# Kernel optimization log

Measured on AMD Instinct MI355X. Metric: run time of the kernel, lower is better.

## Reference

```python
import jax, jax.numpy as jnp
import numpy as np

K = 8                   # num_RQS_bins
MIN_BW = 1e-6; MIN_BH = 1e-6; MIN_D = 1e-6
TAIL = 12.0             # tail_bound for 'linear' tails
# binary masks for num_inputs=4: kept (conditioning) dims and transformed dims per layer
MASK_IDX = [(0, 2), (1, 3), (0, 1), (2, 3)]
INV_IDX = [(1, 3), (0, 2), (2, 3), (0, 1)]


def _rqs_forward(x, uw, uh, ud):
    """Unconstrained rational-quadratic spline, forward (direct) pass.
    x: [B,F]; uw,uh: [B,F,K]; ud: [B,F,K-1]. Returns (y, logabsdet) each [B,F]."""
    const = float(np.log(np.exp(1.0 - MIN_D) - 1.0))
    ud = jnp.pad(ud, ((0, 0), (0, 0), (1, 1)), constant_values=const)  # [B,F,K+1]
    inside = (x >= -TAIL) & (x <= TAIL)
    xc = jnp.clip(x, -TAIL, TAIL)

    widths = MIN_BW + (1.0 - MIN_BW * K) * jax.nn.softmax(uw, -1)
    cumw = jnp.pad(jnp.cumsum(widths, -1), ((0, 0), (0, 0), (1, 0)))
    cumw = 2.0 * TAIL * cumw - TAIL
    cumw = cumw.at[..., 0].set(-TAIL).at[..., -1].set(TAIL)
    widths = cumw[..., 1:] - cumw[..., :-1]

    heights = MIN_BH + (1.0 - MIN_BH * K) * jax.nn.softmax(uh, -1)
    cumh = jnp.pad(jnp.cumsum(heights, -1), ((0, 0), (0, 0), (1, 0)))
    cumh = 2.0 * TAIL * cumh - TAIL
    cumh = cumh.at[..., 0].set(-TAIL).at[..., -1].set(TAIL)
    heights = cumh[..., 1:] - cumh[..., :-1]

    derivs = MIN_D + jax.nn.softplus(ud)  # [B,F,K+1]

    # searchsorted over bin edges (forward mode uses cumwidths)
    idx = jnp.clip(jnp.sum((xc[..., None] >= cumw).astype(jnp.int32), -1) - 1, 0, K - 1)
    g = lambda t: jnp.take_along_axis(t, idx[..., None], axis=-1)[..., 0]
    in_cw, in_w = g(cumw), g(widths)
    in_ch, in_h = g(cumh), g(heights)
    delta = in_h / in_w
    d_k, d_k1 = g(derivs), g(derivs[..., 1:])

    theta = (xc - in_cw) / in_w
    tomt = theta * (1.0 - theta)
    num = in_h * (delta * theta ** 2 + d_k * tomt)
    den = delta + (d_k + d_k1 - 2.0 * delta) * tomt
    y = in_ch + num / den
    dnum = delta ** 2 * (d_k1 * theta ** 2 + 2.0 * delta * tomt + d_k * (1.0 - theta) ** 2)
    lad = jnp.log(dnum) - 2.0 * jnp.log(den)

    return jnp.where(inside, y, x), jnp.where(inside, lad, 0.0)


def setup_inputs() -> dict:
    key = jax.random.key(0)
    ks = jax.random.split(key, 5)
    B, H = 262144, 128
    OM = 3 * K - 1  # 23 params per transformed dim
    inputs = jax.random.normal(ks[0], (B, 4), jnp.float32)
    cond_inputs = jax.random.uniform(ks[1], (B, 1), jnp.float32)
    W1 = jax.random.normal(ks[2], (4, H, 3), jnp.float32) / np.sqrt(3.0)
    b1 = jnp.zeros((4, H), jnp.float32)
    W2 = jax.random.normal(ks[3], (4, H, H), jnp.float32) / np.sqrt(float(H))
    b2 = jnp.zeros((4, H), jnp.float32)
    W3 = jax.random.normal(ks[4], (4, 2 * OM, H), jnp.float32) / np.sqrt(float(H))
    b3 = jnp.zeros((4, 2 * OM), jnp.float32)
    return {"inputs": inputs, "cond_inputs": cond_inputs,
            "W1": W1, "b1": b1, "W2": W2, "b2": b2, "W3": W3, "b3": b3}


def reference(inputs, cond_inputs, W1, b1, W2, b2, W3, b3):
    B = inputs.shape[0]
    x = inputs
    logdets = jnp.zeros((B, 1), dtype=inputs.dtype)
    for l in range(4):  # fixed small number of coupling layers
        midx = list(MASK_IDX[l]); iidx = list(INV_IDX[l])
        m_in = jnp.concatenate([x[:, midx], cond_inputs], -1)  # [B,3]
        h = jax.nn.relu(m_in @ W1[l].T + b1[l])
        h = jax.nn.relu(h @ W2[l].T + b2[l])
        params = h @ W3[l].T + b3[l]  # [B, F*(3K-1)]
        F = len(iidx)
        tp = jnp.swapaxes(params.reshape(B, 3 * K - 1, F), 1, 2)  # [B,F,3K-1]
        y, lad = _rqs_forward(x[:, iidx], tp[..., :K], tp[..., K:2 * K], tp[..., 2 * K:])
        x = x.at[:, iidx].set(y)
        logdets = logdets + jnp.sum(lad, -1, keepdims=True)
    return x, logdets
```

## Files before the change

### kernel.cpp

```cpp
#include <hip/hip_runtime.h>

#define TAILB 12.0f
#define INV2048 4.8828125e-4f

typedef _Float16 half8 __attribute__((ext_vector_type(8)));
typedef _Float16 half4 __attribute__((ext_vector_type(4)));
typedef __fp16 fp16x2 __attribute__((ext_vector_type(2)));
typedef __attribute__((ext_vector_type(4))) float f32x4;

#define MFMAH __builtin_amdgcn_mfma_f32_16x16x32_f16

#define WAVE_SYNC() do {                                  \
    __builtin_amdgcn_sched_barrier(0);                    \
    asm volatile("s_waitcnt lgkmcnt(0)" ::: "memory");    \
    __builtin_amdgcn_sched_barrier(0);                    \
} while (0)

__device__ __forceinline__ float softplus_f(float z) {
    return (z > 15.f) ? z : __logf(1.f + __expf(z));
}

__device__ __forceinline__ void split2h(float v, _Float16& o0, _Float16& o1) {
    _Float16 h0 = (_Float16)v;
    float r1 = v - (float)h0;
    o0 = h0;
    o1 = (_Float16)(r1 * 2048.0f);
}

__device__ __forceinline__ void split4_pk(const float* v, half4& p0, half4& p1) {
    fp16x2 lo = __builtin_amdgcn_cvt_pkrtz(v[0], v[1]);
    fp16x2 hi = __builtin_amdgcn_cvt_pkrtz(v[2], v[3]);
    float r0 = (v[0] - (float)lo.x) * 2048.f;
    float r1 = (v[1] - (float)lo.y) * 2048.f;
    float r2 = (v[2] - (float)hi.x) * 2048.f;
    float r3 = (v[3] - (float)hi.y) * 2048.f;
    fp16x2 rlo = __builtin_amdgcn_cvt_pkrtz(r0, r1);
    fp16x2 rhi = __builtin_amdgcn_cvt_pkrtz(r2, r3);
    p0 = (half4){(_Float16)lo.x, (_Float16)lo.y, (_Float16)hi.x, (_Float16)hi.y};
    p1 = (half4){(_Float16)rlo.x, (_Float16)rlo.y, (_Float16)rhi.x, (_Float16)rhi.y};
}

__global__ __launch_bounds__(256)
void prep_v15(const float* __restrict__ W1, const float* __restrict__ b1,
              const float* __restrict__ W2, const float* __restrict__ W3,
              _Float16* __restrict__ W2F, _Float16* __restrict__ W3F,
              float4* __restrict__ w1p)
{
    int id = blockIdx.x * 256 + threadIdx.x;
    if (id < 65536) {
        int j = id & 7, ln = (id >> 3) & 63, tile = id >> 9;
        int cs = tile & 3, t = (tile >> 2) & 1, wv = (tile >> 3) & 3, l = tile >> 5;
        int n = 32 * wv + 16 * t + (ln & 15);
        int k = 32 * cs + 8 * (ln >> 4) + j;
        _Float16 a, b;
        split2h(W2[l * 16384 + n * 128 + k], a, b);
        W2F[(tile * 2 + 0) * 512 + ln * 8 + j] = a;
        W2F[(tile * 2 + 1) * 512 + ln * 8 + j] = b;
    } else if (id < 90112) {
        int t2 = id - 65536;
        int j = t2 & 7, ln = (t2 >> 3) & 63, tile3 = t2 >> 9;
        int cs = tile3 & 3, q = tile3 >> 2;
        int wv = q % 3, l = q / 3;
        int p = 16 * wv + (ln & 15);
        int n = 32 * cs + 8 * (ln >> 4) + j;
        float v = (p < 46) ? W3[l * 5888 + p * 128 + n] : 0.f;
        _Float16 a, b;
        split2h(v, a, b);
        W3F[(tile3 * 2 + 0) * 512 + ln * 8 + j] = a;
        W3F[(tile3 * 2 + 1) * 512 + ln * 8 + j] = b;
    } else if (id < 90624) {
        int t = id - 90112;
        int l = t >> 7, k = t & 127;
        float4 v;
        v.x = W1[l * 384 + k * 3 + 0];
        v.y = W1[l * 384 + k * 3 + 1];
        v.z = W1[l * 384 + k * 3 + 2];
        v.w = b1[l * 128 + k];
        w1p[t] = v;
    }
}

__global__ __launch_bounds__(64, 2)
void rqs_v15(const float* __restrict__ inp, const float* __restrict__ cond,
             const _Float16* __restrict__ W2F, const _Float16* __restrict__ W3F,
             const float4* __restrict__ w1p,
             const float* __restrict__ b2, const float* __restrict__ b3,
             float* __restrict__ out, int B)
{
    __shared__ __align__(16) _Float16 planes[2][32][128];
    __shared__ float xbuf[32][5];

    char* plw = (char*)&planes[0][0][0];
    const char* pl = plw;

    const int ln   = threadIdx.x;
    const int base = blockIdx.x * 32;
    const int sm   = ln & 15;
    const int qd   = ln >> 4;
    const int s1   = ln & 31;
    const int hi   = ln >> 5;

    int rdaddr[2][4];
    #pragma unroll
    for (int st = 0; st < 2; ++st)
        #pragma unroll
        for (int cs = 0; cs < 4; ++cs)
            rdaddr[st][cs] = (16 * st + sm) * 256 + (((4 * cs + qd) ^ sm) << 4);
    const int wrb = s1 * 256 + hi * 8;

    if (ln < 32) {
        float4 xi = reinterpret_cast<const float4*>(inp)[base + ln];
        xbuf[ln][0] = xi.x; xbuf[ln][1] = xi.y;
        xbuf[ln][2] = xi.z; xbuf[ln][3] = xi.w;
        xbuf[ln][4] = cond[base + ln];
    }
    float ladreg = 0.f;
    WAVE_SYNC();

    #pragma unroll 1
    for (int l = 0; l < 4; ++l) {
        int mi0, mi1, ii0, ii1;
        switch (l) {
            case 0:  mi0 = 0; mi1 = 2; ii0 = 1; ii1 = 3; break;
            case 1:  mi0 = 1; mi1 = 3; ii0 = 0; ii1 = 2; break;
            case 2:  mi0 = 0; mi1 = 1; ii0 = 2; ii1 = 3; break;
            default: mi0 = 2; mi1 = 3; ii0 = 0; ii1 = 1; break;
        }

        {
            float m0 = xbuf[s1][mi0], m1 = xbuf[s1][mi1], cc = xbuf[s1][4];
            const float4* w1l = w1p + l * 128;
            #pragma unroll 4
            for (int g = 0; g < 16; ++g) {
                float v[4];
                #pragma unroll
                for (int j = 0; j < 4; ++j) {
                    float4 w4 = w1l[g * 8 + hi * 4 + j];
                    v[j] = fmaxf(fmaf(w4.x, m0, fmaf(w4.y, m1, fmaf(w4.z, cc, w4.w))), 0.f);
                }
                half4 p0, p1;
                split4_pk(v, p0, p1);
                char* wp = plw + wrb + ((g ^ sm) << 4);
                *(half4*)(wp)        = p0;
                *(half4*)(wp + 8192) = p1;
            }
        }
        WAVE_SYNC();

        half8 bf[2][4][2];
        #pragma unroll
        for (int st = 0; st < 2; ++st)
            #pragma unroll
            for (int cs = 0; cs < 4; ++cs) {
                bf[st][cs][0] = *(const half8*)(pl + rdaddr[st][cs]);
                bf[st][cs][1] = *(const half8*)(pl + rdaddr[st][cs] + 8192);
            }
        WAVE_SYNC();

        const half8* W2F8 = (const half8*)W2F;
        #pragma unroll 1
        for (int np = 0; np < 4; ++np) {
            f32x4 accA[2][2], accB[2][2];
            #pragma unroll
            for (int i = 0; i < 2; ++i) {
                float4 bias = *(const float4*)(b2 + l * 128 + (2 * np + i) * 16 + 4 * qd);
                #pragma unroll
                for (int st = 0; st < 2; ++st) {
                    accA[i][st] = (f32x4){bias.x, bias.y, bias.z, bias.w};
                    accB[i][st] = (f32x4){0.f, 0.f, 0.f, 0.f};
                }
            }
            #pragma unroll
            for (int cs = 0; cs < 4; ++cs) {
                #pragma unroll
                for (int i = 0; i < 2; ++i) {
                    int tile = l * 8 + 2 * np + i;
                    half8 A0 = W2F8[((tile * 4 + cs) * 2 + 0) * 64 + ln];
                    half8 A1 = W2F8[((tile * 4 + cs) * 2 + 1) * 64 + ln];
                    #pragma unroll
                    for (int st = 0; st < 2; ++st) {
                        accA[i][st] = MFMAH(A0, bf[st][cs][0], accA[i][st], 0, 0, 0);
                        accB[i][st] = MFMAH(A0, bf[st][cs][1], accB[i][st], 0, 0, 0);
                        accB[i][st] = MFMAH(A1, bf[st][cs][0], accB[i][st], 0, 0, 0);
                    }
                }
            }
            #pragma unroll
            for (int i = 0; i < 2; ++i) {
                int g = 2 * (2 * np + i) + (qd >> 1);
                #pragma unroll
                for (int st = 0; st < 2; ++st) {
                    float v[4];
                    #pragma unroll
                    for (int r = 0; r < 4; ++r)
                        v[r] = fmaxf(fmaf(INV2048, accB[i][st][r], accA[i][st][r]), 0.f);
                    half4 p0, p1;
                    split4_pk(v, p0, p1);
                    char* wp = plw + (16 * st + sm) * 256 + ((g ^ sm) << 4) + ((qd & 1) << 3);
                    *(half4*)(wp)        = p0;
                    *(half4*)(wp + 8192) = p1;
                }
            }
        }
        WAVE_SYNC();

        #pragma unroll
        for (int st = 0; st < 2; ++st)
            #pragma unroll
            for (int cs = 0; cs < 4; ++cs) {
                bf[st][cs][0] = *(const half8*)(pl + rdaddr[st][cs]);
                bf[st][cs][1] = *(const half8*)(pl + rdaddr[st][cs] + 8192);
            }
        WAVE_SYNC();

        const half8* W3F8 = (const half8*)W3F;
        #pragma unroll 1
        for (int pt = 0; pt < 3; ++pt) {
            f32x4 a3A[2], a3B[2];
            #pragma unroll
            for (int st = 0; st < 2; ++st) {
                a3A[st] = (f32x4){0.f, 0.f, 0.f, 0.f};
                a3B[st] = (f32x4){0.f, 0.f, 0.f, 0.f};
            }
            #pragma unroll
            for (int cs = 0; cs < 4; ++cs) {
                int q = (l * 3 + pt) * 4 + cs;
                half8 A0 = W3F8[(q * 2 + 0) * 64 + ln];
                half8 A1 = W3F8[(q * 2 + 1) * 64 + ln];
                #pragma unroll
                for (int st = 0; st < 2; ++st) {
                    a3A[st] = MFMAH(A0, bf[st][cs][0], a3A[st], 0, 0, 0);
                    a3B[st] = MFMAH(A0, bf[st][cs][1], a3B[st], 0, 0, 0);
                    a3B[st] = MFMAH(A1, bf[st][cs][0], a3B[st], 0, 0, 0);
                }
            }
            #pragma unroll
            for (int st = 0; st < 2; ++st) {
                float4 pv;
                pv.x = fmaf(INV2048, a3B[st][0], a3A[st][0]);
                pv.y = fmaf(INV2048, a3B[st][1], a3A[st][1]);
                pv.z = fmaf(INV2048, a3B[st][2], a3A[st][2]);
                pv.w = fmaf(INV2048, a3B[st][3], a3A[st][3]);
                *(float4*)(plw + (16 * st + sm) * 208 + (16 * pt + 4 * qd) * 4) = pv;
            }
        }
        WAVE_SYNC();

        {
            const float* b3l = b3 + l * 46;
            const float4* prow = (const float4*)(pl + s1 * 208);
            float pr[23];
            #pragma unroll
            for (int i = 0; i < 12; ++i) {
                float4 q = prow[i];
                pr[2 * i] = (hi ? q.y : q.x) + b3l[4 * i + hi];
                if (2 * i + 1 < 23)
                    pr[2 * i + 1] = (hi ? q.w : q.z) + b3l[4 * i + 2 + hi];
            }

            float xin = xbuf[s1][hi == 0 ? ii0 : ii1];

            float d[9];
            d[0] = 1.f; d[8] = 1.f;
            #pragma unroll
            for (int k = 1; k < 8; ++k) d[k] = 1e-6f + softplus_f(pr[16 + k - 1]);

            bool inside = (xin >= -TAILB) && (xin <= TAILB);
            float xc = fminf(fmaxf(xin, -TAILB), TAILB);

            float mw = pr[0], mh = pr[8];
            #pragma unroll
            for (int k = 1; k < 8; ++k) { mw = fmaxf(mw, pr[k]); mh = fmaxf(mh, pr[8 + k]); }
            float ew[8], eh[8], swm = 0.f, shm = 0.f;
            #pragma unroll
            for (int k = 0; k < 8; ++k) {
                ew[k] = __expf(pr[k] - mw);     swm += ew[k];
                eh[k] = __expf(pr[8 + k] - mh); shm += eh[k];
            }
            const float c1 = 1.f - 8e-6f;
            float isw = __fdividef(c1, swm), ish = __fdividef(c1, shm);

            float cum_w = 0.f, cum_h = 0.f;
            float cwk = -TAILB, chk = -TAILB;
            float s_cw = -TAILB, s_w = 2.f * TAILB, s_ch = -TAILB, s_h = 2.f * TAILB;
            float s_d0 = 1.f, s_d1 = d[1];
            #pragma unroll
            for (int k = 0; k < 8; ++k) {
                cum_w += fmaf(ew[k], isw, 1e-6f);
                cum_h += fmaf(eh[k], ish, 1e-6f);
                float cwn = (k == 7) ? TAILB : fmaf(2.f * TAILB, cum_w, -TAILB);
                float chn = (k == 7) ? TAILB : fmaf(2.f * TAILB, cum_h, -TAILB);
                bool ge = (xc >= cwk);
                s_cw = ge ? cwk : s_cw;  s_w = ge ? (cwn - cwk) : s_w;
                s_ch = ge ? chk : s_ch;  s_h = ge ? (chn - chk) : s_h;
                s_d0 = ge ? d[k] : s_d0; s_d1 = ge ? d[k + 1] : s_d1;
                cwk = cwn; chk = chn;
            }

            float rw    = __fdividef(1.f, s_w);
            float th    = (xc - s_cw) * rw;
            float delta = s_h * rw;
            float omt   = 1.f - th;
            float tomt  = th * omt;
            float num   = s_h * fmaf(delta, th * th, s_d0 * tomt);
            float den   = fmaf(s_d0 + s_d1 - 2.f * delta, tomt, delta);
            float y     = s_ch + __fdividef(num, den);
            float dnum  = delta * delta * (s_d1 * th * th + 2.f * delta * tomt + s_d0 * omt * omt);
            float lad   = __logf(dnum) - 2.f * __logf(den);

            xbuf[s1][hi == 0 ? ii0 : ii1] = inside ? y : xin;
            ladreg += inside ? lad : 0.f;
        }
        WAVE_SYNC();
    }

    float lsum = ladreg + __shfl(ladreg, (ln + 32) & 63, 64);
    if (ln < 32) {
        float4 xo;
        xo.x = xbuf[ln][0]; xo.y = xbuf[ln][1];
        xo.z = xbuf[ln][2]; xo.w = xbuf[ln][3];
        reinterpret_cast<float4*>(out)[base + ln] = xo;
        out[(size_t)B * 4 + base + ln] = lsum;
    }
}

extern "C" void kernel_launch(void* const* d_in, const int* in_sizes, int n_in,
                              void* d_out, int out_size, void* d_ws, size_t ws_size,
                              hipStream_t stream) {
    const float* inp  = (const float*)d_in[0];
    const float* cond = (const float*)d_in[1];
    const float* W1   = (const float*)d_in[2];
    const float* b1   = (const float*)d_in[3];
    const float* W2   = (const float*)d_in[4];
    const float* b2   = (const float*)d_in[5];
    const float* W3   = (const float*)d_in[6];
    const float* b3   = (const float*)d_in[7];
    float* out = (float*)d_out;
    int B = in_sizes[0] / 4;

    char* ws = (char*)d_ws;
    _Float16* W2F = (_Float16*)(ws);
    _Float16* W3F = (_Float16*)(ws + 262144);
    float4*   w1p = (float4*)(ws + 360448);

    hipLaunchKernelGGL(prep_v15, dim3(354), dim3(256), 0, stream,
                       W1, b1, W2, W3, W2F, W3F, w1p);
    hipLaunchKernelGGL(rqs_v15, dim3(B / 32), dim3(64), 0, stream,
                       inp, cond, W2F, W3F, w1p, b2, b3, out, B);
}
```

Baseline: 269.5 us.

## Halve LDS staging buffer by processing activations in K-halves, raise occupancy

The 16 KB activation staging buffer becomes 8 KB. The layer-1 output and the layer-2 output are each written and read back in two K-halves, using a row-based XOR swizzle over 128-byte rows. Layer-2 results go into a separate register fragment set (bf3), so the layer-1 fragments do not have to be reloaded. Launch bounds rise from 2 to 3 waves per SIMD to exploit the smaller LDS footprint, at the cost of more wave syncs and tighter register budgets that could cause spills.

```diff
diff --git a/kernel.cpp b/kernel.cpp
--- a/kernel.cpp
+++ b/kernel.cpp
@@ -41,7 +41,7 @@
 }
 
 __global__ __launch_bounds__(256)
-void prep_v15(const float* __restrict__ W1, const float* __restrict__ b1,
+void prep_v16(const float* __restrict__ W1, const float* __restrict__ b1,
               const float* __restrict__ W2, const float* __restrict__ W3,
               _Float16* __restrict__ W2F, _Float16* __restrict__ W3F,
               float4* __restrict__ w1p)
@@ -80,18 +80,18 @@
     }
 }
 
-__global__ __launch_bounds__(64, 2)
-void rqs_v15(const float* __restrict__ inp, const float* __restrict__ cond,
+__global__ __launch_bounds__(64, 3)
+void rqs_v16(const float* __restrict__ inp, const float* __restrict__ cond,
              const _Float16* __restrict__ W2F, const _Float16* __restrict__ W3F,
              const float4* __restrict__ w1p,
              const float* __restrict__ b2, const float* __restrict__ b3,
              float* __restrict__ out, int B)
 {
-    __shared__ __align__(16) _Float16 planes[2][32][128];
+    __shared__ __align__(16) char P[8192];
     __shared__ float xbuf[32][5];
 
-    char* plw = (char*)&planes[0][0][0];
-    const char* pl = plw;
+    char* plw = P;
+    const char* pl = P;
 
     const int ln   = threadIdx.x;
     const int base = blockIdx.x * 32;
@@ -100,13 +100,14 @@
     const int s1   = ln & 31;
     const int hi   = ln >> 5;
 
-    int rdaddr[2][4];
+    int rdK[2][2];
     #pragma unroll
     for (int st = 0; st < 2; ++st)
         #pragma unroll
-        for (int cs = 0; cs < 4; ++cs)
-            rdaddr[st][cs] = (16 * st + sm) * 256 + (((4 * cs + qd) ^ sm) << 4);
-    const int wrb = s1 * 256 + hi * 8;
+        for (int csl = 0; csl < 2; ++csl) {
+            int row = 16 * st + sm;
+            rdK[st][csl] = row * 128 + (((4 * csl + qd) ^ (row & 7)) << 4);
+        }
 
     if (ln < 32) {
         float4 xi = reinterpret_cast<const float4*>(inp)[base + ln];
@@ -127,91 +128,94 @@
             default: mi0 = 2; mi1 = 3; ii0 = 0; ii1 = 1; break;
         }
 
+        half8 bf[2][4][2];
         {
             float m0 = xbuf[s1][mi0], m1 = xbuf[s1][mi1], cc = xbuf[s1][4];
             const float4* w1l = w1p + l * 128;
-            #pragma unroll 4
-            for (int g = 0; g < 16; ++g) {
-                float v[4];
-                #pragma unroll
-                for (int j = 0; j < 4; ++j) {
-                    float4 w4 = w1l[g * 8 + hi * 4 + j];
-                    v[j] = fmaxf(fmaf(w4.x, m0, fmaf(w4.y, m1, fmaf(w4.z, cc, w4.w))), 0.f);
-                }
-                half4 p0, p1;
-                split4_pk(v, p0, p1);
-                char* wp = plw + wrb + ((g ^ sm) << 4);
-                *(half4*)(wp)        = p0;
-                *(half4*)(wp + 8192) = p1;
-            }
-        }
-        WAVE_SYNC();
-
-        half8 bf[2][4][2];
+            #pragma unroll
+            for (int kh = 0; kh < 2; ++kh) {
+                #pragma unroll
+                for (int j4 = 0; j4 < 4; ++j4) {
+                    int gl = 4 * hi + j4;
+                    int g  = 8 * kh + gl;
+                    float v[8];
+                    #pragma unroll
+                    for (int r = 0; r < 8; ++r) {
+                        float4 w4 = w1l[g * 8 + r];
+                        v[r] = fmaxf(fmaf(w4.x, m0, fmaf(w4.y, m1, fmaf(w4.z, cc, w4.w))), 0.f);
+                    }
+                    half4 a0, a1, b0h, b1h;
+                    split4_pk(v, a0, a1);
+                    split4_pk(v + 4, b0h, b1h);
+                    half8 p0 = {a0.x, a0.y, a0.z, a0.w, b0h.x, b0h.y, b0h.z, b0h.w};
+                    half8 p1 = {a1.x, a1.y, a1.z, a1.w, b1h.x, b1h.y, b1h.z, b1h.w};
+                    char* wp = plw + s1 * 128 + ((gl ^ (s1 & 7)) << 4);
+                    *(half8*)(wp)        = p0;
+                    *(half8*)(wp + 4096) = p1;
+                }
+                WAVE_SYNC();
+                #pragma unroll
+                for (int st = 0; st < 2; ++st)
+                    #pragma unroll
+                    for (int csl = 0; csl < 2; ++csl) {
+                        bf[st][2 * kh + csl][0] = *(const half8*)(pl + rdK[st][csl]);
+                        bf[st][2 * kh + csl][1] = *(const half8*)(pl + rdK[st][csl] + 4096);
+                    }
+                WAVE_SYNC();
+            }
+        }
+
+        half8 bf3[2][4][2];
+        const half8* W2F8 = (const half8*)W2F;
         #pragma unroll
-        for (int st = 0; st < 2; ++st)
-            #pragma unroll
-            for (int cs = 0; cs < 4; ++cs) {
-                bf[st][cs][0] = *(const half8*)(pl + rdaddr[st][cs]);
-                bf[st][cs][1] = *(const half8*)(pl + rdaddr[st][cs] + 8192);
-            }
-        WAVE_SYNC();
-
-        const half8* W2F8 = (const half8*)W2F;
-        #pragma unroll 1
-        for (int np = 0; np < 4; ++np) {
-            f32x4 accA[2][2], accB[2][2];
-            #pragma unroll
-            for (int i = 0; i < 2; ++i) {
-                float4 bias = *(const float4*)(b2 + l * 128 + (2 * np + i) * 16 + 4 * qd);
+        for (int ntg = 0; ntg < 2; ++ntg) {
+            #pragma unroll 1
+            for (int ntl = 0; ntl < 4; ++ntl) {
+                int nt = 4 * ntg + ntl;
+                f32x4 accA[2], accB[2];
+                float4 bias = *(const float4*)(b2 + l * 128 + nt * 16 + 4 * qd);
                 #pragma unroll
                 for (int st = 0; st < 2; ++st) {
-                    accA[i][st] = (f32x4){bias.x, bias.y, bias.z, bias.w};
-                    accB[i][st] = (f32x4){0.f, 0.f, 0.f, 0.f};
-                }
-            }
-            #pragma unroll
-            for (int cs = 0; cs < 4; ++cs) {
-                #pragma unroll
-                for (int i = 0; i < 2; ++i) {
-                    int tile = l * 8 + 2 * np + i;
+                    accA[st] = (f32x4){bias.x, bias.y, bias.z, bias.w};
+                    accB[st] = (f32x4){0.f, 0.f, 0.f, 0.f};
+                }
+                #pragma unroll
+                for (int cs = 0; cs < 4; ++cs) {
+                    int tile = l * 8 + nt;
                     half8 A0 = W2F8[((tile * 4 + cs) * 2 + 0) * 64 + ln];
                     half8 A1 = W2F8[((tile * 4 + cs) * 2 + 1) * 64 + ln];
                     #pragma unroll
                     for (int st = 0; st < 2; ++st) {
-                        accA[i][st] = MFMAH(A0, bf[st][cs][0], accA[i][st], 0, 0, 0);
-                        accB[i][st] = MFMAH(A0, bf[st][cs][1], accB[i][st], 0, 0, 0);
-                        accB[i][st] = MFMAH(A1, bf[st][cs][0], accB[i][st], 0, 0, 0);
+                        accA[st] = MFMAH(A0, bf[st][cs][0], accA[st], 0, 0, 0);
+                        accB[st] = MFMAH(A0, bf[st][cs][1], accB[st], 0, 0, 0);
+                        accB[st] = MFMAH(A1, bf[st][cs][0], accB[st], 0, 0, 0);
                     }
                 }
-            }
-            #pragma unroll
-            for (int i = 0; i < 2; ++i) {
-                int g = 2 * (2 * np + i) + (qd >> 1);
                 #pragma unroll
                 for (int st = 0; st < 2; ++st) {
                     float v[4];
                     #pragma unroll
                     for (int r = 0; r < 4; ++r)
-                        v[r] = fmaxf(fmaf(INV2048, accB[i][st][r], accA[i][st][r]), 0.f);
+                        v[r] = fmaxf(fmaf(INV2048, accB[st][r], accA[st][r]), 0.f);
                     half4 p0, p1;
                     split4_pk(v, p0, p1);
-                    char* wp = plw + (16 * st + sm) * 256 + ((g ^ sm) << 4) + ((qd & 1) << 3);
+                    int row = 16 * st + sm;
+                    int gl  = 2 * ntl + (qd >> 1);
+                    char* wp = plw + row * 128 + ((gl ^ (row & 7)) << 4) + ((qd & 1) << 3);
                     *(half4*)(wp)        = p0;
-                    *(half4*)(wp + 8192) = p1;
-                }
-            }
-        }
-        WAVE_SYNC();
-
-        #pragma unroll
-        for (int st = 0; st < 2; ++st)
-            #pragma unroll
-            for (int cs = 0; cs < 4; ++cs) {
-                bf[st][cs][0] = *(const half8*)(pl + rdaddr[st][cs]);
-                bf[st][cs][1] = *(const half8*)(pl + rdaddr[st][cs] + 8192);
-            }
-        WAVE_SYNC();
+                    *(half4*)(wp + 4096) = p1;
+                }
+            }
+            WAVE_SYNC();
+            #pragma unroll
+            for (int st = 0; st < 2; ++st)
+                #pragma unroll
+                for (int csl = 0; csl < 2; ++csl) {
+                    bf3[st][2 * ntg + csl][0] = *(const half8*)(pl + rdK[st][csl]);
+                    bf3[st][2 * ntg + csl][1] = *(const half8*)(pl + rdK[st][csl] + 4096);
+                }
+            WAVE_SYNC();
+        }
 
         const half8* W3F8 = (const half8*)W3F;
         #pragma unroll 1
@@ -229,9 +233,9 @@
                 half8 A1 = W3F8[(q * 2 + 1) * 64 + ln];
                 #pragma unroll
                 for (int st = 0; st < 2; ++st) {
-                    a3A[st] = MFMAH(A0, bf[st][cs][0], a3A[st], 0, 0, 0);
-                    a3B[st] = MFMAH(A0, bf[st][cs][1], a3B[st], 0, 0, 0);
-                    a3B[st] = MFMAH(A1, bf[st][cs][0], a3B[st], 0, 0, 0);
+                    a3A[st] = MFMAH(A0, bf3[st][cs][0], a3A[st], 0, 0, 0);
+                    a3B[st] = MFMAH(A0, bf3[st][cs][1], a3B[st], 0, 0, 0);
+                    a3B[st] = MFMAH(A1, bf3[st][cs][0], a3B[st], 0, 0, 0);
                 }
             }
             #pragma unroll
@@ -343,8 +347,8 @@
     _Float16* W3F = (_Float16*)(ws + 262144);
     float4*   w1p = (float4*)(ws + 360448);
 
-    hipLaunchKernelGGL(prep_v15, dim3(354), dim3(256), 0, stream,
+    hipLaunchKernelGGL(prep_v16, dim3(354), dim3(256), 0, stream,
                        W1, b1, W2, W3, W2F, W3F, w1p);
-    hipLaunchKernelGGL(rqs_v15, dim3(B / 32), dim3(64), 0, stream,
+    hipLaunchKernelGGL(rqs_v16, dim3(B / 32), dim3(64), 0, stream,
                        inp, cond, W2F, W3F, w1p, b2, b3, out, B);
 }
```

Measured after the change: 252.1 us. 6.5% less time.
